# Optimization experiments

Measured on AMD Instinct MI355X. Metric: run time of the kernel, lower is better.

## Reference

```python
import jax, jax.numpy as jnp
import numpy as np

N = 10000        # nodes
E = 640000       # edges (before self-loops)
IN = 128         # in_channels
HID = 32         # hidden_channels
HEADS = 4
HC = HID * HEADS # 128
OUT = 40         # out_channels
NEG_SLOPE = 0.2  # PyG GATConv default


def setup_inputs() -> dict:
    key = jax.random.key(0)
    ks = jax.random.split(key, 12)
    g = lambda k, shape: (jax.random.normal(k, shape, jnp.float32) * 0.1)
    return {
        "x": jax.random.normal(ks[0], (N, IN), jnp.float32),
        "edge_index": jax.random.randint(ks[1], (2, E), 0, N, dtype=jnp.int32),
        # conv1: in -> HID per head, HEADS heads, concat
        "W1": g(ks[2], (IN, HEADS * HID)),
        "a_src1": g(ks[3], (HEADS, HID)),
        "a_dst1": g(ks[4], (HEADS, HID)),
        "b1": jnp.zeros((HEADS * HID,), jnp.float32),
        # conv2: HC -> HC, 1 head
        "W2": g(ks[5], (HC, HC)),
        "a_src2": g(ks[6], (1, HC)),
        "a_dst2": g(ks[7], (1, HC)),
        "b2": jnp.zeros((HC,), jnp.float32),
        # final linear head
        "Wlin": g(ks[8], (HC, OUT)),
        "blin": jnp.zeros((OUT,), jnp.float32),
    }


def _gat_layer(x, W, a_src, a_dst, b, src, dst, heads, n):
    """PyG-style GATConv: gather -> edge attention -> segment softmax -> scatter."""
    d = W.shape[1] // heads
    h = (x @ W).reshape(n, heads, d)                       # [N, H, d]
    asrc = jnp.einsum('nhd,hd->nh', h, a_src)              # [N, H]
    adst = jnp.einsum('nhd,hd->nh', h, a_dst)
    e = jax.nn.leaky_relu(asrc[src] + adst[dst], NEG_SLOPE)  # [E, H]
    m = jax.ops.segment_max(e, dst, num_segments=n)          # per-dst max (stable softmax)
    p = jnp.exp(e - m[dst])
    z = jax.ops.segment_sum(p, dst, num_segments=n)
    alpha = p / (z[dst] + 1e-16)                             # [E, H]
    out = jax.ops.segment_sum(h[src] * alpha[:, :, None], dst, num_segments=n)
    return out.reshape(n, heads * d) + b


def reference(x, edge_index, W1, a_src1, a_dst1, b1, W2, a_src2, a_dst2, b2, Wlin, blin):
    n = x.shape[0]
    loop = jnp.arange(n, dtype=edge_index.dtype)           # add_self_loops=True
    src = jnp.concatenate([edge_index[0], loop])
    dst = jnp.concatenate([edge_index[1], loop])
    # eval mode: dropout is identity
    h1 = jax.nn.elu(_gat_layer(x, W1, a_src1, a_dst1, b1, src, dst, HEADS, n))
    h2 = jax.nn.elu(_gat_layer(h1, W2, a_src2, a_dst2, b2, src, dst, 1, n))
    return h2 @ Wlin + blin
```

## Files before the change

kernel.cpp:

```cpp
#include <hip/hip_runtime.h>
#include <hip/hip_bf16.h>

#define KSUB 8
#define SUBCAP 32
#define CAP 256

using bf16x8 = __attribute__((ext_vector_type(8))) short;
using f32x4  = __attribute__((ext_vector_type(4))) float;

static __device__ __forceinline__ short f2b(float f) {
    __hip_bfloat16 h = __float2bfloat16(f);
    return *reinterpret_cast<short*>(&h);
}

__global__ void build_csr(const int* __restrict__ srcArr, const int* __restrict__ dstArr,
                          int E, int N, int* __restrict__ deg2,
                          unsigned short* __restrict__ csr) {
    int tid = threadIdx.x;
    int k_sub = blockIdx.x & (KSUB - 1);
    int Etot = E + N;
    int base = blockIdx.x * 1024 + tid;
#pragma unroll
    for (int k = 0; k < 4; k++) {
        int i = base + k * 256;
        if (i < Etot) {
            int s, d;
            if (i < E) { s = srcArr[i]; d = dstArr[i]; }
            else       { s = d = i - E; }
            int p = atomicAdd(&deg2[d * KSUB + k_sub], 1);
            if (p < SUBCAP) csr[d * CAP + k_sub * SUBCAP + p] = (unsigned short)s;
        }
    }
}

__global__ __launch_bounds__(256) void prep_w(const float* __restrict__ W1,
                                              const float* __restrict__ W2,
                                              short* __restrict__ Wt1,
                                              short* __restrict__ Wt2) {
    __shared__ float t[32][33];
    int which = blockIdx.x >> 4;
    int tile = blockIdx.x & 15;
    int bi = tile >> 2, bj = tile & 3;
    const float* W = which ? W2 : W1;
    short* Wt = which ? Wt2 : Wt1;
    int tx = threadIdx.x & 31, ty = threadIdx.x >> 5;
#pragma unroll
    for (int i = 0; i < 4; i++) {
        int r = bi * 32 + ty + 8 * i;
        t[ty + 8 * i][tx] = W[r * 128 + bj * 32 + tx];
    }
    __syncthreads();
#pragma unroll
    for (int i = 0; i < 4; i++) {
        int j = bj * 32 + ty + 8 * i;
        Wt[j * 128 + bi * 32 + tx] = f2b(t[tx][ty + 8 * i]);
    }
}

template <int H>
__global__ __launch_bounds__(256) void gemm_mfma(const float* __restrict__ x,
                        const short* __restrict__ Wt,
                        const float* __restrict__ a_src, const float* __restrict__ a_dst,
                        __hip_bfloat16* __restrict__ hwb, float* __restrict__ asrc,
                        float* __restrict__ adst, int N) {
    int wave = (blockIdx.x * 256 + threadIdx.x) >> 6;
    int lane = threadIdx.x & 63;
    int n0 = wave * 16;
    if (n0 >= N) return;
    int m = lane & 15, q = lane >> 4;
    int row = n0 + m;
    bf16x8 afrag[4];
    const float* xr = x + (size_t)row * 128 + q * 8;
#pragma unroll
    for (int kt = 0; kt < 4; kt++) {
        float4 v0 = *(const float4*)(xr + kt * 32);
        float4 v1 = *(const float4*)(xr + kt * 32 + 4);
        bf16x8 f;
        f[0] = f2b(v0.x); f[1] = f2b(v0.y); f[2] = f2b(v0.z); f[3] = f2b(v0.w);
        f[4] = f2b(v1.x); f[5] = f2b(v1.y); f[6] = f2b(v1.z); f[7] = f2b(v1.w);
        afrag[kt] = f;
    }
    float vs[4] = {0.f, 0.f, 0.f, 0.f}, vd[4] = {0.f, 0.f, 0.f, 0.f};
#pragma unroll
    for (int ct = 0; ct < 8; ct++) {
        f32x4 acc = {0.f, 0.f, 0.f, 0.f};
        const short* wrow = Wt + (ct * 16 + m) * 128 + q * 8;
#pragma unroll
        for (int kt = 0; kt < 4; kt++) {
            bf16x8 bfrag = *(const bf16x8*)(wrow + kt * 32);
            acc = __builtin_amdgcn_mfma_f32_16x16x32_bf16(afrag[kt], bfrag, acc, 0, 0, 0);
        }
        int col = ct * 16 + m;
        float asv = a_src[col], adv = a_dst[col];
#pragma unroll
        for (int r = 0; r < 4; r++) {
            int rr = n0 + q * 4 + r;
            hwb[rr * 128 + col] = __float2bfloat16(acc[r]);
            vs[r] += acc[r] * asv;
            vd[r] += acc[r] * adv;
        }
        if (H == 4 && (ct & 1) == 1) {
#pragma unroll
            for (int r = 0; r < 4; r++) {
                float a = vs[r], d = vd[r];
                for (int off = 8; off >= 1; off >>= 1) {
                    a += __shfl_xor(a, off); d += __shfl_xor(d, off);
                }
                if (m == 0) {
                    int rr = n0 + q * 4 + r;
                    asrc[rr * 4 + (ct >> 1)] = a;
                    adst[rr * 4 + (ct >> 1)] = d;
                }
                vs[r] = 0.f; vd[r] = 0.f;
            }
        }
    }
    if (H == 1) {
#pragma unroll
        for (int r = 0; r < 4; r++) {
            float a = vs[r], d = vd[r];
            for (int off = 8; off >= 1; off >>= 1) {
                a += __shfl_xor(a, off); d += __shfl_xor(d, off);
            }
            if (m == 0) {
                int rr = n0 + q * 4 + r;
                asrc[rr] = a;
                adst[rr] = d;
            }
        }
    }
}

__device__ __forceinline__ int slot8(int idx, const int* pref) {
    int k = 0;
#pragma unroll
    for (int j = 1; j < KSUB; j++) k += (idx >= pref[j]);
    return k * SUBCAP + (idx - pref[k]);
}

__global__ __launch_bounds__(64) void agg4(const __hip_bfloat16* __restrict__ hw,
                     const float* __restrict__ asrc, const float* __restrict__ adst,
                     const int* __restrict__ deg2, const unsigned short* __restrict__ csr_src,
                     const float* __restrict__ b, float* __restrict__ y, int N) {
    int n = blockIdx.x;
    int t = threadIdx.x;
    const int4* dp = (const int4*)&deg2[n * KSUB];
    int4 ca = dp[0], cb2 = dp[1];
    int pref[KSUB];
    int cnts[KSUB] = { min(ca.x,SUBCAP), min(ca.y,SUBCAP), min(ca.z,SUBCAP), min(ca.w,SUBCAP),
                       min(cb2.x,SUBCAP), min(cb2.y,SUBCAP), min(cb2.z,SUBCAP), min(cb2.w,SUBCAP) };
    pref[0] = 0;
#pragma unroll
    for (int k = 1; k < KSUB; k++) pref[k] = pref[k-1] + cnts[k-1];
    int deg = pref[KSUB-1] + cnts[KSUB-1];
    const unsigned* hwu = (const unsigned*)hw;
    __shared__ float pe[64 * 4];
    __shared__ int se[64];
    float4 adl = *(const float4*)&adst[n * 4];
    int hcol = t >> 4;
    float2 acc = make_float2(0.f, 0.f);
    float z0 = 0.f, z1 = 0.f, z2 = 0.f, z3 = 0.f;
    for (int base = 0; base < deg; base += 64) {
        int cnt = min(64, deg - base);
        __syncthreads();
        if (t < cnt) {
            int s = (int)csr_src[n * CAP + slot8(base + t, pref)];
            se[t] = s;
            float4 av = *(const float4*)&asrc[s * 4];
            float e0 = av.x + adl.x, e1 = av.y + adl.y;
            float e2 = av.z + adl.z, e3 = av.w + adl.w;
            e0 = e0 > 0.f ? e0 : 0.2f * e0;
            e1 = e1 > 0.f ? e1 : 0.2f * e1;
            e2 = e2 > 0.f ? e2 : 0.2f * e2;
            e3 = e3 > 0.f ? e3 : 0.2f * e3;
            float p0 = __expf(e0), p1 = __expf(e1), p2 = __expf(e2), p3 = __expf(e3);
            pe[t * 4 + 0] = p0; pe[t * 4 + 1] = p1;
            pe[t * 4 + 2] = p2; pe[t * 4 + 3] = p3;
            z0 += p0; z1 += p1; z2 += p2; z3 += p3;
        } else {
            se[t] = 0;
            pe[t * 4 + 0] = 0.f; pe[t * 4 + 1] = 0.f;
            pe[t * 4 + 2] = 0.f; pe[t * 4 + 3] = 0.f;
        }
        __syncthreads();
#pragma unroll
        for (int cb = 0; cb < 64; cb += 16) {
            if (cb < cnt) {
#pragma unroll
                for (int u = 0; u < 16; u++) {
                    int c = cb + u;
                    int s = se[c];
                    float p = pe[c * 4 + hcol];
                    unsigned v = hwu[s * 64 + t];
                    acc.x += p * __uint_as_float(v << 16);
                    acc.y += p * __uint_as_float(v & 0xffff0000u);
                }
            }
        }
    }
    for (int off = 32; off >= 1; off >>= 1) {
        z0 += __shfl_xor(z0, off); z1 += __shfl_xor(z1, off);
        z2 += __shfl_xor(z2, off); z3 += __shfl_xor(z3, off);
    }
    float z = (hcol == 0) ? z0 : (hcol == 1) ? z1 : (hcol == 2) ? z2 : z3;
    float inv = 1.f / (z + 1e-16f);
    float2 bb = *(const float2*)&b[t * 2];
    float r0 = acc.x * inv + bb.x;
    float r1 = acc.y * inv + bb.y;
    r0 = r0 > 0.f ? r0 : (__expf(r0) - 1.0f);
    r1 = r1 > 0.f ? r1 : (__expf(r1) - 1.0f);
    *(float2*)&y[n * 128 + t * 2] = make_float2(r0, r1);
}

__global__ __launch_bounds__(64) void agg1_lin(const __hip_bfloat16* __restrict__ hw,
                         const float* __restrict__ asrc, const float* __restrict__ adst,
                         const int* __restrict__ deg2, const unsigned short* __restrict__ csr_src,
                         const float* __restrict__ b, const float* __restrict__ Wl,
                         const float* __restrict__ bl, float* __restrict__ out,
                         int N, int OUTC) {
    int n = blockIdx.x;
    int t = threadIdx.x;
    const int4* dp = (const int4*)&deg2[n * KSUB];
    int4 ca = dp[0], cb2 = dp[1];
    int pref[KSUB];
    int cnts[KSUB] = { min(ca.x,SUBCAP), min(ca.y,SUBCAP), min(ca.z,SUBCAP), min(ca.w,SUBCAP),
                       min(cb2.x,SUBCAP), min(cb2.y,SUBCAP), min(cb2.z,SUBCAP), min(cb2.w,SUBCAP) };
    pref[0] = 0;
#pragma unroll
    for (int k = 1; k < KSUB; k++) pref[k] = pref[k-1] + cnts[k-1];
    int deg = pref[KSUB-1] + cnts[KSUB-1];
    const unsigned* hwu = (const unsigned*)hw;
    __shared__ float pe[64];
    __shared__ int se[64];
    __shared__ float yrow[128];
    float adl = adst[n];
    float2 acc = make_float2(0.f, 0.f);
    float zp = 0.f;
    for (int base = 0; base < deg; base += 64) {
        int cnt = min(64, deg - base);
        __syncthreads();
        if (t < cnt) {
            int s = (int)csr_src[n * CAP + slot8(base + t, pref)];
            se[t] = s;
            float e = asrc[s] + adl;
            e = e > 0.f ? e : 0.2f * e;
            float p = __expf(e);
            pe[t] = p;
            zp += p;
        } else {
            se[t] = 0;
            pe[t] = 0.f;
        }
        __syncthreads();
#pragma unroll
        for (int cb = 0; cb < 64; cb += 16) {
            if (cb < cnt) {
#pragma unroll
                for (int u = 0; u < 16; u++) {
                    int c = cb + u;
                    int s = se[c];
                    float p = pe[c];
                    unsigned v = hwu[s * 64 + t];
                    acc.x += p * __uint_as_float(v << 16);
                    acc.y += p * __uint_as_float(v & 0xffff0000u);
                }
            }
        }
    }
    for (int off = 32; off >= 1; off >>= 1) zp += __shfl_xor(zp, off);
    float inv = 1.f / (zp + 1e-16f);
    float2 bb = *(const float2*)&b[t * 2];
    float r0 = acc.x * inv + bb.x;
    float r1 = acc.y * inv + bb.y;
    r0 = r0 > 0.f ? r0 : (__expf(r0) - 1.0f);
    r1 = r1 > 0.f ? r1 : (__expf(r1) - 1.0f);
    yrow[t * 2] = r0; yrow[t * 2 + 1] = r1;
    __syncthreads();
    if (t < OUTC) {
        float a = bl[t];
        for (int k = 0; k < 128; k++) a += yrow[k] * Wl[k * OUTC + t];
        out[n * OUTC + t] = a;
    }
}

extern "C" void kernel_launch(void* const* d_in, const int* in_sizes, int n_in,
                              void* d_out, int out_size, void* d_ws, size_t ws_size,
                              hipStream_t stream) {
    const float* x       = (const float*)d_in[0];
    const int*   ei      = (const int*)d_in[1];
    const float* W1      = (const float*)d_in[2];
    const float* a_src1  = (const float*)d_in[3];
    const float* a_dst1  = (const float*)d_in[4];
    const float* b1      = (const float*)d_in[5];
    const float* W2      = (const float*)d_in[6];
    const float* a_src2  = (const float*)d_in[7];
    const float* a_dst2  = (const float*)d_in[8];
    const float* b2      = (const float*)d_in[9];
    const float* Wlin    = (const float*)d_in[10];
    const float* blin    = (const float*)d_in[11];
    float* out = (float*)d_out;

    const int N = in_sizes[0] / 128;
    const int E = in_sizes[1] / 2;
    const int OUTC = in_sizes[10] / 128;
    const int Etot = E + N;
    const int* src = ei;
    const int* dst = ei + E;
    const int NCB = (Etot + 1023) / 1024;
    const int NGB = (N / 16 + 3) / 4;

    char* w = (char*)d_ws;
    size_t off = 0;
    auto alloc = [&](size_t bytes) -> char* {
        char* p = w + off;
        off += (bytes + 255) & ~(size_t)255;
        return p;
    };
    int*             deg2  = (int*)alloc((size_t)N * KSUB * 4);
    unsigned short*  csr   = (unsigned short*)alloc((size_t)N * CAP * 2);
    __hip_bfloat16*  hwb   = (__hip_bfloat16*)alloc((size_t)N * 128 * 2);
    float*           bufY  = (float*)alloc((size_t)N * 128 * 4);
    short*           Wt1   = (short*)alloc((size_t)128 * 128 * 2);
    short*           Wt2   = (short*)alloc((size_t)128 * 128 * 2);
    float*           asrc1 = (float*)alloc((size_t)N * 4 * 4);
    float*           adst1 = (float*)alloc((size_t)N * 4 * 4);
    float*           asrc2 = (float*)alloc((size_t)N * 4);
    float*           adst2 = (float*)alloc((size_t)N * 4);
    (void)ws_size;

    hipMemsetAsync(deg2, 0, (size_t)N * KSUB * 4, stream);
    prep_w<<<32, 256, 0, stream>>>(W1, W2, Wt1, Wt2);
    build_csr<<<NCB, 256, 0, stream>>>(src, dst, E, N, deg2, csr);

    gemm_mfma<4><<<NGB, 256, 0, stream>>>(x, Wt1, a_src1, a_dst1, hwb, asrc1, adst1, N);
    agg4<<<N, 64, 0, stream>>>(hwb, asrc1, adst1, deg2, csr, b1, bufY, N);

    gemm_mfma<1><<<NGB, 256, 0, stream>>>(bufY, Wt2, a_src2, a_dst2, hwb, asrc2, adst2, N);
    agg1_lin<<<N, 64, 0, stream>>>(hwb, asrc2, adst2, deg2, csr, b2, Wlin, blin, out, N, OUTC);
}
```

Measured before the change: 181.2 us.

## Process four edges per wave with 16-byte row loads in GAT aggregation

The two aggregation kernels now split the 64-lane wave into four edge groups of 16 lanes. Each lane loads a uint4 (8 bf16 values) of the source row instead of one 32-bit word, and the four partial sums are combined with cross-lane shuffles at the end. The edge staging chunk grows from 64 to 128 so most nodes need one staging pass. The aim is more memory-level parallelism and wider loads per gather. In exchange, the inner loop is no longer unrolled, and the per-lane register array is indexed dynamically at the end, which may push it to scratch memory.

```diff
diff --git a/kernel.cpp b/kernel.cpp
--- a/kernel.cpp
+++ b/kernel.cpp
@@ -12,6 +12,8 @@
     __hip_bfloat16 h = __float2bfloat16(f);
     return *reinterpret_cast<short*>(&h);
 }
+static __device__ __forceinline__ float blo(unsigned u) { return __uint_as_float(u << 16); }
+static __device__ __forceinline__ float bhi(unsigned u) { return __uint_as_float(u & 0xffff0000u); }
 
 __global__ void build_csr(const int* __restrict__ srcArr, const int* __restrict__ dstArr,
                           int E, int N, int* __restrict__ deg2,
@@ -144,6 +146,9 @@
                      const float* __restrict__ b, float* __restrict__ y, int N) {
     int n = blockIdx.x;
     int t = threadIdx.x;
+    int er = t >> 4;
+    int cg = t & 15;
+    int hcol = cg >> 2;
     const int4* dp = (const int4*)&deg2[n * KSUB];
     int4 ca = dp[0], cb2 = dp[1];
     int pref[KSUB];
@@ -153,50 +158,49 @@
 #pragma unroll
     for (int k = 1; k < KSUB; k++) pref[k] = pref[k-1] + cnts[k-1];
     int deg = pref[KSUB-1] + cnts[KSUB-1];
-    const unsigned* hwu = (const unsigned*)hw;
-    __shared__ float pe[64 * 4];
-    __shared__ int se[64];
+    const uint4* hw4 = (const uint4*)hw;
+    __shared__ float pe[128 * 4];
+    __shared__ int se[128];
     float4 adl = *(const float4*)&adst[n * 4];
-    int hcol = t >> 4;
-    float2 acc = make_float2(0.f, 0.f);
+    float acc[8] = {0.f,0.f,0.f,0.f,0.f,0.f,0.f,0.f};
     float z0 = 0.f, z1 = 0.f, z2 = 0.f, z3 = 0.f;
-    for (int base = 0; base < deg; base += 64) {
-        int cnt = min(64, deg - base);
+    for (int base = 0; base < deg; base += 128) {
+        int cnt = min(128, deg - base);
         __syncthreads();
-        if (t < cnt) {
-            int s = (int)csr_src[n * CAP + slot8(base + t, pref)];
-            se[t] = s;
-            float4 av = *(const float4*)&asrc[s * 4];
-            float e0 = av.x + adl.x, e1 = av.y + adl.y;
-            float e2 = av.z + adl.z, e3 = av.w + adl.w;
-            e0 = e0 > 0.f ? e0 : 0.2f * e0;
-            e1 = e1 > 0.f ? e1 : 0.2f * e1;
-            e2 = e2 > 0.f ? e2 : 0.2f * e2;
-            e3 = e3 > 0.f ? e3 : 0.2f * e3;
-            float p0 = __expf(e0), p1 = __expf(e1), p2 = __expf(e2), p3 = __expf(e3);
-            pe[t * 4 + 0] = p0; pe[t * 4 + 1] = p1;
-            pe[t * 4 + 2] = p2; pe[t * 4 + 3] = p3;
-            z0 += p0; z1 += p1; z2 += p2; z3 += p3;
-        } else {
-            se[t] = 0;
-            pe[t * 4 + 0] = 0.f; pe[t * 4 + 1] = 0.f;
-            pe[t * 4 + 2] = 0.f; pe[t * 4 + 3] = 0.f;
+#pragma unroll
+        for (int rep = 0; rep < 2; rep++) {
+            int idx = t + 64 * rep;
+            if (idx < cnt) {
+                int s = (int)csr_src[n * CAP + slot8(base + idx, pref)];
+                se[idx] = s;
+                float4 av = *(const float4*)&asrc[s * 4];
+                float e0 = av.x + adl.x, e1 = av.y + adl.y;
+                float e2 = av.z + adl.z, e3 = av.w + adl.w;
+                e0 = e0 > 0.f ? e0 : 0.2f * e0;
+                e1 = e1 > 0.f ? e1 : 0.2f * e1;
+                e2 = e2 > 0.f ? e2 : 0.2f * e2;
+                e3 = e3 > 0.f ? e3 : 0.2f * e3;
+                float p0 = __expf(e0), p1 = __expf(e1), p2 = __expf(e2), p3 = __expf(e3);
+                pe[idx * 4 + 0] = p0; pe[idx * 4 + 1] = p1;
+                pe[idx * 4 + 2] = p2; pe[idx * 4 + 3] = p3;
+                z0 += p0; z1 += p1; z2 += p2; z3 += p3;
+            }
         }
         __syncthreads();
-#pragma unroll
-        for (int cb = 0; cb < 64; cb += 16) {
-            if (cb < cnt) {
-#pragma unroll
-                for (int u = 0; u < 16; u++) {
-                    int c = cb + u;
-                    int s = se[c];
-                    float p = pe[c * 4 + hcol];
-                    unsigned v = hwu[s * 64 + t];
-                    acc.x += p * __uint_as_float(v << 16);
-                    acc.y += p * __uint_as_float(v & 0xffff0000u);
-                }
-            }
-        }
+        for (int c = er; c < cnt; c += 4) {
+            int s = se[c];
+            float p = pe[c * 4 + hcol];
+            uint4 v = hw4[s * 16 + cg];
+            acc[0] += p * blo(v.x); acc[1] += p * bhi(v.x);
+            acc[2] += p * blo(v.y); acc[3] += p * bhi(v.y);
+            acc[4] += p * blo(v.z); acc[5] += p * bhi(v.z);
+            acc[6] += p * blo(v.w); acc[7] += p * bhi(v.w);
+        }
+    }
+#pragma unroll
+    for (int i = 0; i < 8; i++) {
+        acc[i] += __shfl_xor(acc[i], 16);
+        acc[i] += __shfl_xor(acc[i], 32);
     }
     for (int off = 32; off >= 1; off >>= 1) {
         z0 += __shfl_xor(z0, off); z1 += __shfl_xor(z1, off);
@@ -204,12 +208,13 @@
     }
     float z = (hcol == 0) ? z0 : (hcol == 1) ? z1 : (hcol == 2) ? z2 : z3;
     float inv = 1.f / (z + 1e-16f);
-    float2 bb = *(const float2*)&b[t * 2];
-    float r0 = acc.x * inv + bb.x;
-    float r1 = acc.y * inv + bb.y;
+    int col = cg * 8 + er * 2;
+    float2 bb = *(const float2*)&b[col];
+    float r0 = acc[er * 2]     * inv + bb.x;
+    float r1 = acc[er * 2 + 1] * inv + bb.y;
     r0 = r0 > 0.f ? r0 : (__expf(r0) - 1.0f);
     r1 = r1 > 0.f ? r1 : (__expf(r1) - 1.0f);
-    *(float2*)&y[n * 128 + t * 2] = make_float2(r0, r1);
+    *(float2*)&y[n * 128 + col] = make_float2(r0, r1);
 }
 
 __global__ __launch_bounds__(64) void agg1_lin(const __hip_bfloat16* __restrict__ hw,
@@ -220,6 +225,8 @@
                          int N, int OUTC) {
     int n = blockIdx.x;
     int t = threadIdx.x;
+    int er = t >> 4;
+    int cg = t & 15;
     const int4* dp = (const int4*)&deg2[n * KSUB];
     int4 ca = dp[0], cb2 = dp[1];
     int pref[KSUB];
@@ -229,52 +236,54 @@
 #pragma unroll
     for (int k = 1; k < KSUB; k++) pref[k] = pref[k-1] + cnts[k-1];
     int deg = pref[KSUB-1] + cnts[KSUB-1];
-    const unsigned* hwu = (const unsigned*)hw;
-    __shared__ float pe[64];
-    __shared__ int se[64];
+    const uint4* hw4 = (const uint4*)hw;
+    __shared__ float pe[128];
+    __shared__ int se[128];
     __shared__ float yrow[128];
     float adl = adst[n];
-    float2 acc = make_float2(0.f, 0.f);
+    float acc[8] = {0.f,0.f,0.f,0.f,0.f,0.f,0.f,0.f};
     float zp = 0.f;
-    for (int base = 0; base < deg; base += 64) {
-        int cnt = min(64, deg - base);
+    for (int base = 0; base < deg; base += 128) {
+        int cnt = min(128, deg - base);
         __syncthreads();
-        if (t < cnt) {
-            int s = (int)csr_src[n * CAP + slot8(base + t, pref)];
-            se[t] = s;
-            float e = asrc[s] + adl;
-            e = e > 0.f ? e : 0.2f * e;
-            float p = __expf(e);
-            pe[t] = p;
-            zp += p;
-        } else {
-            se[t] = 0;
-            pe[t] = 0.f;
+#pragma unroll
+        for (int rep = 0; rep < 2; rep++) {
+            int idx = t + 64 * rep;
+            if (idx < cnt) {
+                int s = (int)csr_src[n * CAP + slot8(base + idx, pref)];
+                se[idx] = s;
+                float e = asrc[s] + adl;
+                e = e > 0.f ? e : 0.2f * e;
+                float p = __expf(e);
+                pe[idx] = p;
+                zp += p;
+            }
         }
         __syncthreads();
-#pragma unroll
-        for (int cb = 0; cb < 64; cb += 16) {
-            if (cb < cnt) {
-#pragma unroll
-                for (int u = 0; u < 16; u++) {
-                    int c = cb + u;
-                    int s = se[c];
-                    float p = pe[c];
-                    unsigned v = hwu[s * 64 + t];
-                    acc.x += p * __uint_as_float(v << 16);
-                    acc.y += p * __uint_as_float(v & 0xffff0000u);
-                }
-            }
-        }
+        for (int c = er; c < cnt; c += 4) {
+            int s = se[c];
+            float p = pe[c];
+            uint4 v = hw4[s * 16 + cg];
+            acc[0] += p * blo(v.x); acc[1] += p * bhi(v.x);
+            acc[2] += p * blo(v.y); acc[3] += p * bhi(v.y);
+            acc[4] += p * blo(v.z); acc[5] += p * bhi(v.z);
+            acc[6] += p * blo(v.w); acc[7] += p * bhi(v.w);
+        }
+    }
+#pragma unroll
+    for (int i = 0; i < 8; i++) {
+        acc[i] += __shfl_xor(acc[i], 16);
+        acc[i] += __shfl_xor(acc[i], 32);
     }
     for (int off = 32; off >= 1; off >>= 1) zp += __shfl_xor(zp, off);
     float inv = 1.f / (zp + 1e-16f);
-    float2 bb = *(const float2*)&b[t * 2];
-    float r0 = acc.x * inv + bb.x;
-    float r1 = acc.y * inv + bb.y;
+    int col = cg * 8 + er * 2;
+    float2 bb = *(const float2*)&b[col];
+    float r0 = acc[er * 2]     * inv + bb.x;
+    float r1 = acc[er * 2 + 1] * inv + bb.y;
     r0 = r0 > 0.f ? r0 : (__expf(r0) - 1.0f);
     r1 = r1 > 0.f ? r1 : (__expf(r1) - 1.0f);
-    yrow[t * 2] = r0; yrow[t * 2 + 1] = r1;
+    yrow[col] = r0; yrow[col + 1] = r1;
     __syncthreads();
     if (t < OUTC) {
         float a = bl[t];
```

Measured after the change: 172.2 us. 5.0% less time.
